# Optimization experiments

Hardware: AMD Instinct MI355X
Metric: run time of the kernel (lower is better)

The kernel has to match this reference:

```python
import jax, jax.numpy as jnp
import numpy as np

DC_WZ = 15
ETA = 0.1
RADIUS = DC_WZ // 2  # 7
EPS = 1e-3


def avg_pool2d(x, k, pad):
    # torch F.avg_pool2d default: zero padding, count_include_pad=True -> divide by k*k always
    s = jax.lax.reduce_window(
        x, 0.0, jax.lax.add,
        window_dimensions=(1, 1, k, k),
        window_strides=(1, 1, 1, 1),
        padding=[(0, 0), (0, 0), (pad, pad), (pad, pad)])
    return s / float(k * k)


def min_pool2d_replicate(x, k, pad):
    # replicate (edge) pad then VALID min-pool, matching -max_pool2d(-pad(x, replicate))
    xp = jnp.pad(x, ((0, 0), (0, 0), (pad, pad), (pad, pad)), mode='edge')
    return jax.lax.reduce_window(
        xp, jnp.inf, jax.lax.min,
        window_dimensions=(1, 1, k, k),
        window_strides=(1, 1, 1, 1),
        padding='VALID')


def guided_filter(guide, src, radius, eps=EPS):
    k = 2 * radius + 1
    mean_I = avg_pool2d(guide, k, radius)
    mean_p = avg_pool2d(src, k, radius)
    mean_Ip = avg_pool2d(guide * src, k, radius)
    cov_Ip = mean_Ip - mean_I * mean_p
    mean_II = avg_pool2d(guide * guide, k, radius)
    var_I = mean_II - mean_I * mean_I
    a = cov_Ip / (var_I + eps)
    b = mean_p - a * mean_I
    mean_a = avg_pool2d(a, k, radius)
    mean_b = avg_pool2d(b, k, radius)
    return mean_a * guide + mean_b


def setup_inputs() -> dict:
    key = jax.random.key(0)
    k1, k2 = jax.random.split(key)
    smoky_image = jax.random.uniform(k1, (16, 3, 512, 512), dtype=jnp.float32)
    rho_DNN = jax.random.uniform(k2, (16, 3, 512, 512), dtype=jnp.float32)
    return {"smoky_image": smoky_image, "rho_DNN": rho_DNN}


def reference(smoky_image, rho_DNN):
    # dark channel: per-pixel min over RGB, then 15x15 min-pool with replicate pad
    dc_pixel = jnp.min(smoky_image, axis=-3, keepdims=True)  # [B,1,H,W]
    dc_coarse = min_pool2d_replicate(dc_pixel, DC_WZ, RADIUS)
    guide_I = jnp.mean(smoky_image, axis=-3, keepdims=True)
    dc_refined = guided_filter(guide_I, dc_coarse, RADIUS, EPS)
    dc_refined = jax.lax.stop_gradient(dc_refined)  # torch: no_grad + detach
    dc_rho = (ETA + dc_refined) / (ETA + 1.0) * (1.0 - rho_DNN)
    return smoky_image - dc_rho
```

## Files before the change

kernel.cpp:

```cpp
#include <hip/hip_runtime.h>

#define BATCH 16
#define HH 512
#define WW 512
#define PLANE (HH*WW)

#define LDS_WAIT()   asm volatile("s_waitcnt lgkmcnt(0)" ::: "memory")
#define WAVE_FENCE() asm volatile("" ::: "memory")

__device__ __forceinline__ float bf_lo(unsigned u) {
    union { unsigned u; float f; } c; c.u = u << 16; return c.f;
}
__device__ __forceinline__ float bf_hi(unsigned u) {
    union { unsigned u; float f; } c; c.u = u & 0xFFFF0000u; return c.f;
}
__device__ __forceinline__ unsigned f2bf(float f) {
    union { float f; unsigned u; } c; c.f = f;
    return (c.u + 0x7FFFu + ((c.u >> 16) & 1u)) >> 16;
}
__device__ __forceinline__ unsigned packbf(float x, float y) {
    return f2bf(x) | (f2bf(y) << 16);
}
__device__ __forceinline__ float min3f(float a, float b, float c) {
    return fminf(fminf(a, b), c);
}
__device__ __forceinline__ float4 add4(float4 a, float4 b) {
    return make_float4(a.x+b.x, a.y+b.y, a.z+b.z, a.w+b.w);
}
__device__ __forceinline__ float4 tsum15v(const float4* p) {
    float4 s = add4(add4(add4(p[0],p[1]),add4(p[2],p[3])),
                    add4(add4(p[4],p[5]),add4(p[6],p[7])));
    float4 u = add4(add4(add4(p[8],p[9]),add4(p[10],p[11])),
                    add4(add4(p[12],p[13]),p[14]));
    return add4(s, u);
}

#define T1 64
#define HALO 7
#define LW (T1 + 2*HALO)

__global__ __launch_bounds__(256) void k1_guide_minpool(
    const float* __restrict__ smoky, unsigned* __restrict__ gp)
{
    __shared__ float dcp[LW*LW];
    __shared__ float vmn[T1*LW];
    __shared__ unsigned short gsh[T1*T1];
    int nwg = gridDim.x;
    int wg = (blockIdx.x & 7) * (nwg >> 3) + (blockIdx.x >> 3);
    int img  = wg >> 6;
    int tile = wg & 63;
    int y0 = (tile >> 3) * T1;
    int x0 = (tile & 7) * T1;
    int t = threadIdx.x;
    const float* s0 = smoky + (size_t)img * 3 * PLANE;
    unsigned* gpl = gp + (size_t)img * PLANE;

    for (int i = t; i < LW*LW; i += 256) {
        int ly = i / LW, lx = i - ly * LW;
        int iy = y0 - HALO + ly, ix = x0 - HALO + lx;
        int cy = min(max(iy, 0), HH-1);
        int cx = min(max(ix, 0), WW-1);
        const float* bp = s0 + cy * WW + cx;
        float c0 = bp[0], c1 = bp[PLANE], c2 = bp[2*PLANE];
        dcp[i] = min3f(c0, c1, c2);
        if (ly >= HALO && ly < HALO+T1 && lx >= HALO && lx < HALO+T1)
            gsh[(ly-HALO)*T1 + (lx-HALO)] = (unsigned short)f2bf((c0 + c1 + c2) * (1.0f/3.0f));
    }
    __syncthreads();
    for (int i = t; i < T1*LW; i += 256) {
        int r = i / LW, c = i - r * LW;
        const float* q = &dcp[r*LW + c];
        float m = min3f(min3f(min3f(q[0*LW],q[1*LW],q[2*LW]),
                              min3f(q[3*LW],q[4*LW],q[5*LW]),
                              min3f(q[6*LW],q[7*LW],q[8*LW])),
                        min3f(q[9*LW],q[10*LW],q[11*LW]),
                        min3f(q[12*LW],q[13*LW],q[14*LW]));
        vmn[i] = m;
    }
    __syncthreads();
    for (int i = t; i < T1*T1; i += 256) {
        int r = i >> 6, c = i & 63;
        const float* q = &vmn[r*LW + c];
        float m = min3f(min3f(min3f(q[0],q[1],q[2]),
                              min3f(q[3],q[4],q[5]),
                              min3f(q[6],q[7],q[8])),
                        min3f(q[9],q[10],q[11]),
                        min3f(q[12],q[13],q[14]));
        gpl[(y0+r)*WW + x0 + c] = (unsigned)gsh[r*T1+c] | (f2bf(m) << 16);
    }
}

#define RS2 16

__global__ __launch_bounds__(256) void k2_ab(
    const unsigned* __restrict__ gp, unsigned* __restrict__ abO)
{
    __shared__ float4 ls[4][2][80];
    int nwg = gridDim.x;
    int wg = (blockIdx.x & 7) * (nwg >> 3) + (blockIdx.x >> 3);
    int w = threadIdx.x >> 6, l = threadIdx.x & 63;
    int gw = wg * 4 + w;
    int img   = gw >> 8;
    int cg    = (gw >> 5) & 7;
    int strip = gw & 31;
    int y0 = strip * RS2;
    int c0 = cg * 64;
    const unsigned* gpP = gp + (size_t)img * PLANE;
    unsigned* abP = abO + (size_t)img * PLANE;

    int col0 = c0 - 7 + l;
    int col1 = c0 + 57 + l;
    bool v0 = (col0 >= 0);
    bool v1 = (l < 14) && (col1 < WW);

    float sI0=0,sII0=0,sP0=0,sIp0=0;
    float sI1=0,sII1=0,sP1=0,sIp1=0;

    auto loadrow = [&](int y, unsigned& u0, unsigned& u1) {
        int yc = min(max(y, 0), HH-1);
        const unsigned* r = gpP + (size_t)yc * WW;
        unsigned a = 0u, b = 0u;
        if (v0) a = r[col0];
        if (v1) b = r[col1];
        bool rv = ((unsigned)y < (unsigned)HH);
        u0 = rv ? a : 0u;
        u1 = rv ? b : 0u;
    };

    for (int r = y0 - 8; r <= y0 + 6; ++r) {
        unsigned u0,u1; loadrow(r, u0,u1);
        float g0=bf_lo(u0), p0=bf_hi(u0), g1=bf_lo(u1), p1=bf_hi(u1);
        sI0+=g0; sII0+=g0*g0; sP0+=p0; sIp0+=g0*p0;
        sI1+=g1; sII1+=g1*g1; sP1+=p1; sIp1+=g1*p1;
    }
    unsigned a1M,a1H, s1M,s1H, a2M,a2H, s2M,s2H;
    loadrow(y0 + 7, a1M, a1H);
    loadrow(y0 - 8, s1M, s1H);
    loadrow(y0 + 8, a2M, a2H);
    loadrow(y0 - 7, s2M, s2H);

    float4* Le = &ls[w][0][0];
    float4* Lo = &ls[w][1][0];
    const float inv225 = 1.0f/225.0f;

    for (int y = y0; y < y0 + RS2; y += 2) {
        {
            float gA=bf_lo(a1M), pA=bf_hi(a1M), gS=bf_lo(s1M), pS=bf_hi(s1M);
            sI0 += gA-gS; sII0 += gA*gA-gS*gS; sP0 += pA-pS; sIp0 += gA*pA-gS*pS;
            float gAh=bf_lo(a1H), pAh=bf_hi(a1H), gSh=bf_lo(s1H), pSh=bf_hi(s1H);
            sI1 += gAh-gSh; sII1 += gAh*gAh-gSh*gSh; sP1 += pAh-pSh; sIp1 += gAh*pAh-gSh*pSh;
        }
        float eI0=sI0, eII0=sII0, eP0=sP0, eIp0=sIp0;
        float eI1=sI1, eII1=sII1, eP1=sP1, eIp1=sIp1;
        {
            float gA=bf_lo(a2M), pA=bf_hi(a2M), gS=bf_lo(s2M), pS=bf_hi(s2M);
            sI0 += gA-gS; sII0 += gA*gA-gS*gS; sP0 += pA-pS; sIp0 += gA*pA-gS*pS;
            float gAh=bf_lo(a2H), pAh=bf_hi(a2H), gSh=bf_lo(s2H), pSh=bf_hi(s2H);
            sI1 += gAh-gSh; sII1 += gAh*gAh-gSh*gSh; sP1 += pAh-pSh; sIp1 += gAh*pAh-gSh*pSh;
        }
        loadrow(y + 9,  a1M, a1H);
        loadrow(y - 6,  s1M, s1H);
        loadrow(y + 10, a2M, a2H);
        loadrow(y - 5,  s2M, s2H);
        Le[l] = make_float4(eI0, eII0, eP0, eIp0);
        Lo[l] = make_float4(sI0, sII0, sP0, sIp0);
        if (l < 14) {
            Le[64+l] = make_float4(eI1, eII1, eP1, eIp1);
            Lo[64+l] = make_float4(sI1, sII1, sP1, sIp1);
        }
        LDS_WAIT();
        float4 Te = tsum15v(&Le[l]);
        float4 To = tsum15v(&Lo[l]);
        WAVE_FENCE();
        {
            float mI = Te.x*inv225, mP = Te.z*inv225;
            float va = (Te.w*inv225 - mI*mP) / (Te.y*inv225 - mI*mI + 1e-3f);
            abP[(size_t)y*WW + c0 + l] = packbf(va, mP - va*mI);
        }
        {
            float mI = To.x*inv225, mP = To.z*inv225;
            float va = (To.w*inv225 - mI*mP) / (To.y*inv225 - mI*mI + 1e-3f);
            abP[(size_t)(y+1)*WW + c0 + l] = packbf(va, mP - va*mI);
        }
    }
}

__global__ __launch_bounds__(256) void k3_final(
    const unsigned* __restrict__ abI,
    const float* __restrict__ smoky, const float* __restrict__ rho,
    float* __restrict__ out)
{
    __shared__ float4 ls[4][80];
    int nwg = gridDim.x;
    int wg = (blockIdx.x & 7) * (nwg >> 3) + (blockIdx.x >> 3);
    int w = threadIdx.x >> 6, l = threadIdx.x & 63;
    int gw = wg * 4 + w;
    int img   = gw >> 8;
    int cg    = (gw >> 5) & 7;
    int strip = gw & 31;
    int y0 = strip * RS2;
    int c0 = cg * 64;
    const unsigned* abP = abI + (size_t)img * PLANE;
    const float* sP = smoky + (size_t)img * 3 * PLANE;
    const float* rP = rho   + (size_t)img * 3 * PLANE;
    float* oP = out + (size_t)img * 3 * PLANE;

    int col0 = c0 - 7 + l;
    int col1 = c0 + 57 + l;
    bool v0 = (col0 >= 0);
    bool v1 = (l < 14) && (col1 < WW);

    float sa0=0, sb0=0, sa1=0, sb1=0;

    auto loadrow = [&](int y, unsigned& u0, unsigned& u1) {
        int yc = min(max(y, 0), HH-1);
        const unsigned* r = abP + (size_t)yc * WW;
        unsigned a = 0u, b = 0u;
        if (v0) a = r[col0];
        if (v1) b = r[col1];
        bool rv = ((unsigned)y < (unsigned)HH);
        u0 = rv ? a : 0u;
        u1 = rv ? b : 0u;
    };

    for (int r = y0 - 8; r <= y0 + 6; ++r) {
        unsigned u0,u1; loadrow(r, u0,u1);
        sa0 += bf_lo(u0); sb0 += bf_hi(u0);
        sa1 += bf_lo(u1); sb1 += bf_hi(u1);
    }
    unsigned a1M,a1H, s1M,s1H, a2M,a2H, s2M,s2H;
    loadrow(y0 + 7, a1M, a1H);
    loadrow(y0 - 8, s1M, s1H);
    loadrow(y0 + 8, a2M, a2H);
    loadrow(y0 - 7, s2M, s2H);

    float esA0,esA1,esA2, erA0,erA1,erA2;
    float esB0,esB1,esB2, erB0,erB1,erB2;
    int yend = y0 + RS2;
    auto loademit = [&](int y,
                        float& e0, float& e1, float& e2,
                        float& r0, float& r1, float& r2) {
        int e = min(y, yend - 1);
        size_t off = (size_t)e*WW + c0 + l;
        e0 = sP[off]; e1 = sP[off+PLANE]; e2 = sP[off+2*PLANE];
        r0 = rP[off]; r1 = rP[off+PLANE]; r2 = rP[off+2*PLANE];
    };
    loademit(y0,     esA0,esA1,esA2, erA0,erA1,erA2);
    loademit(y0 + 1, esB0,esB1,esB2, erB0,erB1,erB2);

    float4* L4 = &ls[w][0];
    const float inv225 = 1.0f/225.0f;
    const float inv11  = 1.0f/1.1f;
    const float third  = 1.0f/3.0f;
    for (int y = y0; y < yend; y += 2) {
        sa0 += bf_lo(a1M) - bf_lo(s1M);  sb0 += bf_hi(a1M) - bf_hi(s1M);
        sa1 += bf_lo(a1H) - bf_lo(s1H);  sb1 += bf_hi(a1H) - bf_hi(s1H);
        float ea0=sa0, eb0=sb0, ea1=sa1, eb1=sb1;
        sa0 += bf_lo(a2M) - bf_lo(s2M);  sb0 += bf_hi(a2M) - bf_hi(s2M);
        sa1 += bf_lo(a2H) - bf_lo(s2H);  sb1 += bf_hi(a2H) - bf_hi(s2H);
        float cA0=esA0, cA1=esA1, cA2=esA2, dA0=erA0, dA1=erA1, dA2=erA2;
        float cB0=esB0, cB1=esB1, cB2=esB2, dB0=erB0, dB1=erB1, dB2=erB2;
        loadrow(y + 9,  a1M, a1H);
        loadrow(y - 6,  s1M, s1H);
        loadrow(y + 10, a2M, a2H);
        loadrow(y - 5,  s2M, s2H);
        loademit(y + 2, esA0,esA1,esA2, erA0,erA1,erA2);
        loademit(y + 3, esB0,esB1,esB2, erB0,erB1,erB2);
        L4[l] = make_float4(ea0, eb0, sa0, sb0);
        if (l < 14) L4[64+l] = make_float4(ea1, eb1, sa1, sb1);
        LDS_WAIT();
        float4 T = tsum15v(&L4[l]);
        WAVE_FENCE();
        {
            float g = (cA0 + cA1 + cA2) * third;
            float f = (0.1f + T.x*inv225*g + T.y*inv225) * inv11;
            size_t off = (size_t)y*WW + c0 + l;
            oP[off]          = cA0 - f*(1.0f - dA0);
            oP[off+PLANE]    = cA1 - f*(1.0f - dA1);
            oP[off+2*PLANE]  = cA2 - f*(1.0f - dA2);
        }
        {
            float g = (cB0 + cB1 + cB2) * third;
            float f = (0.1f + T.z*inv225*g + T.w*inv225) * inv11;
            size_t off = (size_t)(y+1)*WW + c0 + l;
            oP[off]          = cB0 - f*(1.0f - dB0);
            oP[off+PLANE]    = cB1 - f*(1.0f - dB1);
            oP[off+2*PLANE]  = cB2 - f*(1.0f - dB2);
        }
    }
}

extern "C" void kernel_launch(void* const* d_in, const int* in_sizes, int n_in,
                              void* d_out, int out_size, void* d_ws, size_t ws_size,
                              hipStream_t stream) {
    const float* smoky = (const float*)d_in[0];
    const float* rho   = (const float*)d_in[1];
    float* out = (float*)d_out;
    const size_t P = (size_t)BATCH * PLANE;
    unsigned* gpbuf = (unsigned*)d_ws;
    unsigned* abbuf = (unsigned*)d_ws + P;

    k1_guide_minpool<<<BATCH*64, 256, 0, stream>>>(smoky, gpbuf);
    k2_ab<<<BATCH*64, 256, 0, stream>>>(gpbuf, abbuf);
    k3_final<<<BATCH*64, 256, 0, stream>>>(abbuf, smoky, rho, out);
}
```

Measured before the change: 76.49 us.

## Split k3 into box-filter phase then fully unrolled batched output phase

The final kernel first runs the sliding box filter over the strip and stores the per-row mean_a/mean_b as packed bf16 in LDS. A second, fully unrolled loop then reads all 16 rows' smoky and rho values and writes the outputs, so many global loads are in flight at once instead of being software-pipelined two rows ahead. Launch bounds now request 4 blocks per CU. This adds LDS usage and extra bf16 rounding of the mean coefficients, and raises register pressure in the unrolled loop.

```diff
diff --git a/kernel.cpp b/kernel.cpp
--- a/kernel.cpp
+++ b/kernel.cpp
@@ -185,12 +185,13 @@
     }
 }
 
-__global__ __launch_bounds__(256) void k3_final(
+__global__ __launch_bounds__(256, 4) void k3_final(
     const unsigned* __restrict__ abI,
     const float* __restrict__ smoky, const float* __restrict__ rho,
     float* __restrict__ out)
 {
     __shared__ float4 ls[4][80];
+    __shared__ unsigned mbuf[4][16][64];
     int nwg = gridDim.x;
     int wg = (blockIdx.x & 7) * (nwg >> 3) + (blockIdx.x >> 3);
     int w = threadIdx.x >> 6, l = threadIdx.x & 63;
@@ -234,59 +235,49 @@
     loadrow(y0 + 8, a2M, a2H);
     loadrow(y0 - 7, s2M, s2H);
 
-    float esA0,esA1,esA2, erA0,erA1,erA2;
-    float esB0,esB1,esB2, erB0,erB1,erB2;
-    int yend = y0 + RS2;
-    auto loademit = [&](int y,
-                        float& e0, float& e1, float& e2,
-                        float& r0, float& r1, float& r2) {
-        int e = min(y, yend - 1);
-        size_t off = (size_t)e*WW + c0 + l;
-        e0 = sP[off]; e1 = sP[off+PLANE]; e2 = sP[off+2*PLANE];
-        r0 = rP[off]; r1 = rP[off+PLANE]; r2 = rP[off+2*PLANE];
-    };
-    loademit(y0,     esA0,esA1,esA2, erA0,erA1,erA2);
-    loademit(y0 + 1, esB0,esB1,esB2, erB0,erB1,erB2);
-
     float4* L4 = &ls[w][0];
+    unsigned (*mb)[64] = mbuf[w];
     const float inv225 = 1.0f/225.0f;
-    const float inv11  = 1.0f/1.1f;
-    const float third  = 1.0f/3.0f;
-    for (int y = y0; y < yend; y += 2) {
+
+    for (int y = y0; y < y0 + RS2; y += 2) {
         sa0 += bf_lo(a1M) - bf_lo(s1M);  sb0 += bf_hi(a1M) - bf_hi(s1M);
         sa1 += bf_lo(a1H) - bf_lo(s1H);  sb1 += bf_hi(a1H) - bf_hi(s1H);
         float ea0=sa0, eb0=sb0, ea1=sa1, eb1=sb1;
         sa0 += bf_lo(a2M) - bf_lo(s2M);  sb0 += bf_hi(a2M) - bf_hi(s2M);
         sa1 += bf_lo(a2H) - bf_lo(s2H);  sb1 += bf_hi(a2H) - bf_hi(s2H);
-        float cA0=esA0, cA1=esA1, cA2=esA2, dA0=erA0, dA1=erA1, dA2=erA2;
-        float cB0=esB0, cB1=esB1, cB2=esB2, dB0=erB0, dB1=erB1, dB2=erB2;
         loadrow(y + 9,  a1M, a1H);
         loadrow(y - 6,  s1M, s1H);
         loadrow(y + 10, a2M, a2H);
         loadrow(y - 5,  s2M, s2H);
-        loademit(y + 2, esA0,esA1,esA2, erA0,erA1,erA2);
-        loademit(y + 3, esB0,esB1,esB2, erB0,erB1,erB2);
         L4[l] = make_float4(ea0, eb0, sa0, sb0);
         if (l < 14) L4[64+l] = make_float4(ea1, eb1, sa1, sb1);
         LDS_WAIT();
         float4 T = tsum15v(&L4[l]);
         WAVE_FENCE();
-        {
-            float g = (cA0 + cA1 + cA2) * third;
-            float f = (0.1f + T.x*inv225*g + T.y*inv225) * inv11;
-            size_t off = (size_t)y*WW + c0 + l;
-            oP[off]          = cA0 - f*(1.0f - dA0);
-            oP[off+PLANE]    = cA1 - f*(1.0f - dA1);
-            oP[off+2*PLANE]  = cA2 - f*(1.0f - dA2);
-        }
-        {
-            float g = (cB0 + cB1 + cB2) * third;
-            float f = (0.1f + T.z*inv225*g + T.w*inv225) * inv11;
-            size_t off = (size_t)(y+1)*WW + c0 + l;
-            oP[off]          = cB0 - f*(1.0f - dB0);
-            oP[off+PLANE]    = cB1 - f*(1.0f - dB1);
-            oP[off+2*PLANE]  = cB2 - f*(1.0f - dB2);
-        }
+        int i = y - y0;
+        mb[i][l]   = packbf(T.x*inv225, T.y*inv225);
+        mb[i+1][l] = packbf(T.z*inv225, T.w*inv225);
+    }
+    LDS_WAIT();
+
+    unsigned mr[16];
+    #pragma unroll
+    for (int i = 0; i < 16; ++i) mr[i] = mb[i][l];
+    LDS_WAIT();
+    WAVE_FENCE();
+
+    const float inv11 = 1.0f/1.1f;
+    const float third = 1.0f/3.0f;
+    #pragma unroll
+    for (int i = 0; i < 16; ++i) {
+        size_t off = (size_t)(y0 + i)*WW + c0 + l;
+        float s0 = sP[off], s1 = sP[off+PLANE], s2 = sP[off+2*PLANE];
+        float r0 = rP[off], r1 = rP[off+PLANE], r2 = rP[off+2*PLANE];
+        float g = (s0 + s1 + s2) * third;
+        float f = (0.1f + bf_lo(mr[i])*g + bf_hi(mr[i])) * inv11;
+        oP[off]          = s0 - f*(1.0f - r0);
+        oP[off+PLANE]    = s1 - f*(1.0f - r1);
+        oP[off+2*PLANE]  = s2 - f*(1.0f - r2);
     }
 }
 
```

Result: no change. 77.79 us (+1.7%).
